# Kernel tuning notes

Hardware: AMD Instinct MI355X
Metric: run time of the kernel (lower is better)

## Reference

```python
import jax, jax.numpy as jnp
import numpy as np

DIM = 512
NUM_HEADS = 16
WIN = (7, 7)
N = WIN[0] * WIN[1]          # 49 tokens per window
NW = 64                      # windows per image
B = 32                       # images
B_ = B * NW                  # total windows = 2048
SCALE = (DIM // NUM_HEADS) ** -0.5


def _relative_position_index(wh, ww):
    coords = np.stack(np.meshgrid(np.arange(wh), np.arange(ww), indexing='ij'))  # (2, wh, ww)
    coords = coords.reshape(2, -1)                                               # (2, N)
    rel = coords[:, :, None] - coords[:, None, :]                                # (2, N, N)
    rel = rel.transpose(1, 2, 0).astype(np.int32)                                # (N, N, 2)
    rel[:, :, 0] += wh - 1
    rel[:, :, 1] += ww - 1
    rel[:, :, 0] *= 2 * ww - 1
    return jnp.asarray(rel.sum(-1), dtype=jnp.int32)                             # (N, N)


def _shift_mask(nw, n):
    # Swin-style additive mask: 0 within groups, -100 across groups.
    rng = np.random.RandomState(0)
    groups = rng.randint(0, 4, size=(nw, n)).astype(np.int32)
    m = np.where(groups[:, :, None] == groups[:, None, :], 0.0, -100.0)
    return jnp.asarray(m, dtype=jnp.float32)                                     # (nW, N, N)


def setup_inputs() -> dict:
    key = jax.random.key(0)
    ks = jax.random.split(key, 5)
    x = jax.random.normal(ks[0], (B_, N, DIM), dtype=jnp.float32)
    qkv_w = jax.random.normal(ks[1], (3 * DIM, DIM), dtype=jnp.float32) * 0.02
    qkv_b = jnp.zeros((3 * DIM,), dtype=jnp.float32)
    proj_w = jax.random.normal(ks[2], (DIM, DIM), dtype=jnp.float32) * 0.02
    proj_b = jnp.zeros((DIM,), dtype=jnp.float32)
    rpb_table = jax.random.normal(ks[3], ((2 * WIN[0] - 1) * (2 * WIN[1] - 1), NUM_HEADS), dtype=jnp.float32) * 0.02
    mask = _shift_mask(NW, N)
    rel_idx = _relative_position_index(*WIN)
    return {"x": x, "mask": mask, "qkv_w": qkv_w, "qkv_b": qkv_b,
            "proj_w": proj_w, "proj_b": proj_b, "rpb_table": rpb_table,
            "rel_idx": rel_idx}


def reference(x, mask, qkv_w, qkv_b, proj_w, proj_b, rpb_table, rel_idx):
    b_, n, c = x.shape
    nh = rpb_table.shape[1]
    d = c // nh
    # qkv projection: (B_, N, 3, nH, d) -> q, k, v each (B_, nH, N, d)
    qkv = (jnp.einsum('bnc,oc->bno', x, qkv_w) + qkv_b).reshape(b_, n, 3, nh, d)
    qkv = jnp.transpose(qkv, (2, 0, 3, 1, 4))
    q, k, v = qkv[0], qkv[1], qkv[2]
    attn = jnp.einsum('bhnd,bhmd->bhnm', q * SCALE, k)                     # (B_, nH, N, N)
    # gathered relative position bias: (N*N, nH) -> (nH, N, N)
    bias = rpb_table[rel_idx.reshape(-1)].reshape(n, n, nh)
    attn = attn + jnp.transpose(bias, (2, 0, 1))[None]
    # shifted-window mask add
    nw = mask.shape[0]
    attn = attn.reshape(b_ // nw, nw, nh, n, n) + mask[None, :, None]
    attn = attn.reshape(b_, nh, n, n)
    attn = jax.nn.softmax(attn, axis=-1)
    out = jnp.einsum('bhnm,bhmd->bhnd', attn, v)                           # (B_, nH, N, d)
    out = jnp.transpose(out, (0, 2, 1, 3)).reshape(b_, n, c)
    return jnp.einsum('bnc,oc->bno', out, proj_w) + proj_b
```

## Files before the change

### kernel.cpp

```cpp
#include <hip/hip_runtime.h>
#include <hip/hip_bf16.h>
#include <stdint.h>
#include <stddef.h>

#define B_TOT   2048
#define NTOK    49
#define CDIM    512
#define NHEAD   16
#define HD      32
#define NWIN    64
#define MROWS   (B_TOT*NTOK)
#define O_QKV   1536
#define SCALE_F 0.17677669529663687f

typedef short bf16x8 __attribute__((ext_vector_type(8)));
typedef float f32x4  __attribute__((ext_vector_type(4)));

__device__ __forceinline__ unsigned short f2bf(float f){
  union { float f; unsigned u; } v; v.f = f;
  unsigned r = v.u + 0x7fffu + ((v.u >> 16) & 1u);
  return (unsigned short)(r >> 16);
}

#define GL16(g,l) __builtin_amdgcn_global_load_lds( \
      (const __attribute__((address_space(1))) unsigned int*)(g), \
      (__attribute__((address_space(3))) unsigned int*)(l), 16, 0, 0)

__global__ void k_cvt_x(const float* __restrict__ x, unsigned short* __restrict__ xb, int n4){
  int i = blockIdx.x * blockDim.x + threadIdx.x;
  int st = gridDim.x * blockDim.x;
  for (; i < n4; i += st){
    float4 v = ((const float4*)x)[i];
    uint2 o;
    o.x = (unsigned)f2bf(v.x) | ((unsigned)f2bf(v.y) << 16);
    o.y = (unsigned)f2bf(v.z) | ((unsigned)f2bf(v.w) << 16);
    ((uint2*)xb)[i] = o;
  }
}

__global__ void k_prep(const float* __restrict__ qkv_w, const float* __restrict__ proj_w,
                       const float* __restrict__ rpb, const int* __restrict__ rel_idx,
                       const float* __restrict__ mask,
                       unsigned short* __restrict__ wqkv, unsigned short* __restrict__ wproj,
                       float* __restrict__ bmb){
  int i = blockIdx.x * blockDim.x + threadIdx.x;
  int st = gridDim.x * blockDim.x;
  for (int j = i; j < O_QKV*CDIM; j += st) wqkv[j] = f2bf(qkv_w[j]);
  for (int j = i; j < CDIM*CDIM;  j += st) wproj[j] = f2bf(proj_w[j]);
  const int TOT = NWIN * NHEAD * NTOK * 64;
  for (int j = i; j < TOT; j += st){
    int wh  = j / (NTOK*64);
    int rem = j - wh * (NTOK*64);
    int qt  = rem >> 6, kt = rem & 63;
    int wi = wh >> 4, h = wh & 15;
    float v;
    if (kt < NTOK){
      int rc = qt * NTOK + kt;
      v = mask[wi * (NTOK*NTOK) + rc] + rpb[rel_idx[rc] * NHEAD + h];
    } else v = -1e30f;
    bmb[j] = v;
  }
}

#define LDA_(P,RG,MI,S) (*(const bf16x8*)(rA + (P)*32768 + (RG)*16384 + (MI)*2048 + ((S)?(cb0^64):cb0)))
#define LDB_(P,CG,NI,S) (*(const bf16x8*)(rB + (P)*32768 + (CG)*16384 + (NI)*2048 + ((S)?(cb0^64):cb0)))

#define STAGE_A(P,HG,KT) { \
    GL16(aS0 + (size_t)(HG)*64*Kb + (size_t)(KT)*128, ldA + (P)*32768 + (HG)*16384); \
    GL16(aS1 + (size_t)(HG)*64*Kb + (size_t)(KT)*128, ldA + (P)*32768 + (HG)*16384 + 8192); }
#define STAGE_B(P,HG,KT) { \
    GL16(bS0 + (size_t)(HG)*32*Kb + (size_t)(KT)*128, ldB + (P)*32768 + (HG)*16384); \
    GL16(bS1 + (size_t)(HG)*32*Kb + (size_t)(KT)*128, ldB + (P)*32768 + (HG)*16384 + 8192); }

#define PHASE(P,RG,CG,DOA,DOB,VM,...) { \
  if (DOA){ _Pragma("unroll") for (int mi=0;mi<4;++mi){ af[mi][0]=LDA_(P,RG,mi,0); af[mi][1]=LDA_(P,RG,mi,1);} } \
  if (DOB){ _Pragma("unroll") for (int ni=0;ni<2;++ni){ bf_[ni][0]=LDB_(P,CG,ni,0); bf_[ni][1]=LDB_(P,CG,ni,1);} } \
  __VA_ARGS__; \
  __builtin_amdgcn_s_barrier(); \
  asm volatile("s_waitcnt lgkmcnt(0)" ::: "memory"); \
  __builtin_amdgcn_sched_barrier(0); \
  __builtin_amdgcn_s_setprio(1); \
  _Pragma("unroll") for (int s=0;s<2;++s) \
    _Pragma("unroll") for (int mi=0;mi<4;++mi) \
      _Pragma("unroll") for (int ni=0;ni<2;++ni) \
        acc[(RG)*4+mi][(CG)*2+ni] = __builtin_amdgcn_mfma_f32_16x16x32_bf16(af[mi][s], bf_[ni][s], acc[(RG)*4+mi][(CG)*2+ni], 0,0,0); \
  __builtin_amdgcn_s_setprio(0); \
  if (VM) asm volatile("s_waitcnt vmcnt(4)" ::: "memory"); \
  __builtin_amdgcn_s_barrier(); \
  asm volatile("" ::: "memory"); \
}

template<int OUT_F32>
__global__ __launch_bounds__(512, 2) void k_gemm8(const unsigned short* __restrict__ Ag,
                                                  const unsigned short* __restrict__ Bg,
                                                  const float* __restrict__ bias,
                                                  void* __restrict__ Cout,
                                                  int Ndim, int Kdim){
  extern __shared__ char smem[];
  const int tid = threadIdx.x;
  const int wv = tid >> 6, lane = tid & 63, lg = lane >> 4, lr = lane & 15;
  const int wm = wv >> 2, wn = wv & 3;

  const int nbx = gridDim.x;
  const int nwg = nbx * gridDim.y;
  const int id  = blockIdx.y * nbx + blockIdx.x;
  const int nid = (id & 7) * (nwg >> 3) + (id >> 3);
  const int bx = nid % nbx, by = nid / nbx;
  const int bm0 = by * 256, bn0 = bx * 256;
  const size_t Kb = (size_t)Kdim * 2;
  const int NIT = Kdim >> 7;

  const int srow = tid >> 3;
  const int scb  = ((tid & 7) << 4) ^ ((srow & 7) << 4);
  const char* aS0 = (const char*)Ag + (size_t)(bm0 + srow) * Kb + scb;
  const char* aS1 = (const char*)Ag + (size_t)(bm0 + 128 + srow) * Kb + scb;
  const char* bS0 = (const char*)Bg + (size_t)(bn0 + (srow>>5)*64 + (srow&31)) * Kb + scb;
  const char* bS1 = (const char*)Bg + (size_t)(bn0 + 128 + (srow>>5)*64 + (srow&31)) * Kb + scb;
  char* ldA = smem + wv * 1024;
  char* ldB = smem + 65536 + wv * 1024;

  const int cb0 = (lg * 16) ^ ((lr & 7) << 4);
  const char* rA = smem + (wm*64 + lr) * 128;
  const char* rB = smem + 65536 + (wn*32 + lr) * 128;

  f32x4 acc[8][4];
  #pragma unroll
  for (int i = 0; i < 8; ++i)
    #pragma unroll
    for (int j = 0; j < 4; ++j)
      #pragma unroll
      for (int r = 0; r < 4; ++r) acc[i][j][r] = 0.f;

  bf16x8 af[4][2], bf_[2][2];

  STAGE_A(0,0,0); STAGE_A(0,1,0); STAGE_B(0,0,0); STAGE_B(0,1,0);
  STAGE_A(1,0,1); STAGE_B(1,1,1);
  asm volatile("s_waitcnt vmcnt(4)" ::: "memory");
  __builtin_amdgcn_s_barrier();
  asm volatile("" ::: "memory");

  for (int it = 0; it < NIT; ++it){
    const int T = 2*it;
    PHASE(0, 0,0, 1,1, 0, STAGE_A(1,1,(T+1)))
    PHASE(0, 0,1, 0,1, 0, STAGE_B(1,0,(T+1)))
    PHASE(0, 1,1, 1,0, 0, STAGE_A(0,0,(T+2)))
    PHASE(0, 1,0, 0,1, 1, STAGE_B(0,1,(T+2)))
    PHASE(1, 0,0, 1,1, 0, STAGE_A(0,1,(T+2)))
    PHASE(1, 0,1, 0,1, 0, STAGE_B(0,0,(T+2)))
    PHASE(1, 1,1, 1,0, 0, STAGE_A(1,0,(T+3)))
    PHASE(1, 1,0, 0,1, 1, STAGE_B(1,1,(T+3)))
  }

  #pragma unroll
  for (int RG = 0; RG < 2; ++RG)
    #pragma unroll
    for (int mi = 0; mi < 4; ++mi)
      #pragma unroll
      for (int CG = 0; CG < 2; ++CG)
        #pragma unroll
        for (int ni = 0; ni < 2; ++ni){
          f32x4 v = acc[RG*4+mi][CG*2+ni];
          const int col = bn0 + wn*64 + CG*32 + ni*16 + lr;
          const float bc = bias[col];
          #pragma unroll
          for (int r = 0; r < 4; ++r){
            const int row = bm0 + wm*128 + RG*64 + mi*16 + lg*4 + r;
            const float t = v[r] + bc;
            if (OUT_F32) ((float*)Cout)[(size_t)row * Ndim + col] = t;
            else ((unsigned short*)Cout)[(size_t)row * Ndim + col] = f2bf(t);
          }
        }
}

__global__ __launch_bounds__(256) void k_attn(const unsigned short* __restrict__ qkv,
                                              const float* __restrict__ bm,
                                              unsigned short* __restrict__ ao){
  __shared__ char lds[4][12288];
  const int wv = threadIdx.x >> 6, lane = threadIdx.x & 63;
  const int lg = lane >> 4, lr = lane & 15;
  const int gw = blockIdx.x * 4 + wv;
  const int w = gw >> 4, h = gw & 15, wi = w & (NWIN - 1);
  char* Vt = lds[wv];
  char* P  = lds[wv] + 4096;

  const unsigned short* base = qkv + (size_t)w * NTOK * O_QKV + h * HD;

  const int vkt = lane >> 2, vch = lane & 3;
  bf16x8 vld[4];
  #pragma unroll
  for (int t = 0; t < 4; ++t){
    int kt = 16*t + vkt; int kts = kt < NTOK ? kt : NTOK-1;
    vld[t] = *(const bf16x8*)(base + 1024 + (size_t)kts * O_QKV + vch * 8);
  }

  bf16x8 qf[4], kf[4];
  #pragma unroll
  for (int i = 0; i < 4; ++i){
    int t = 16*i + lr; int ts = t < NTOK ? t : NTOK-1;
    qf[i] = *(const bf16x8*)(base + (size_t)ts * O_QKV + lg*8);
    kf[i] = *(const bf16x8*)(base + 512 + (size_t)ts * O_QKV + lg*8);
  }

  const float* bmp = bm + (size_t)(wi * NHEAD + h) * (NTOK * 64);
  f32x4 bias[4][4];
  #pragma unroll
  for (int mi = 0; mi < 4; ++mi){
    int qt = 16*mi + lr; int qtc = qt < NTOK ? qt : NTOK-1;
    #pragma unroll
    for (int ni = 0; ni < 4; ++ni)
      bias[mi][ni] = *(const f32x4*)(bmp + qtc*64 + ni*16 + lg*4);
  }

  f32x4 z4 = {0.f, 0.f, 0.f, 0.f};
  f32x4 s2[4][4];
  #pragma unroll
  for (int ni = 0; ni < 4; ++ni)
    #pragma unroll
    for (int mi = 0; mi < 4; ++mi)
      s2[ni][mi] = __builtin_amdgcn_mfma_f32_16x16x32_bf16(kf[ni], qf[mi], z4, 0, 0, 0);

  #pragma unroll
  for (int t = 0; t < 4; ++t){
    int kt = 16*t + vkt;
    #pragma unroll
    for (int j = 0; j < 8; ++j){
      int d = vch*8 + j;
      int swz = ((d & 7) ^ (d >> 3)) & 7;
      int byte = d*128 + ((2*kt) ^ (swz << 4));
      *(unsigned short*)(Vt + byte) = (unsigned short)vld[t][j];
    }
  }

  #pragma unroll
  for (int mi = 0; mi < 4; ++mi){
    float v[4][4];
    float mx = -1e30f;
    #pragma unroll
    for (int ni = 0; ni < 4; ++ni)
      #pragma unroll
      for (int r = 0; r < 4; ++r){
        float t = s2[ni][mi][r] * SCALE_F + bias[mi][ni][r];
        v[ni][r] = t;
        mx = fmaxf(mx, t);
      }
    mx = fmaxf(mx, __shfl_xor(mx, 16));
    mx = fmaxf(mx, __shfl_xor(mx, 32));
    float sum = 0.f;
    #pragma unroll
    for (int ni = 0; ni < 4; ++ni)
      #pragma unroll
      for (int r = 0; r < 4; ++r){
        float p = __expf(v[ni][r] - mx);
        v[ni][r] = p;
        sum += p;
      }
    sum += __shfl_xor(sum, 16);
    sum += __shfl_xor(sum, 32);
    float rn = 1.0f / sum;
    const int qt = 16*mi + lr;
    #pragma unroll
    for (int ni = 0; ni < 4; ++ni){
      unsigned p0 = (unsigned)f2bf(v[ni][0]*rn) | ((unsigned)f2bf(v[ni][1]*rn) << 16);
      unsigned p1 = (unsigned)f2bf(v[ni][2]*rn) | ((unsigned)f2bf(v[ni][3]*rn) << 16);
      uint2 pw; pw.x = p0; pw.y = p1;
      int byte = qt*128 + ((32*ni + 8*lg) ^ ((lr & 7) << 4));
      *(uint2*)(P + byte) = pw;
    }
  }

  f32x4 o[4][2];
  #pragma unroll
  for (int mi = 0; mi < 4; ++mi)
    #pragma unroll
    for (int ni = 0; ni < 2; ++ni)
      #pragma unroll
      for (int r = 0; r < 4; ++r) o[mi][ni][r] = 0.f;

  #pragma unroll
  for (int s = 0; s < 2; ++s){
    bf16x8 pf[4], vf[2];
    #pragma unroll
    for (int mi = 0; mi < 4; ++mi)
      pf[mi] = *(const bf16x8*)(P + (16*mi + lr)*128 + ((64*s + 16*lg) ^ ((lr & 7) << 4)));
    #pragma unroll
    for (int ni = 0; ni < 2; ++ni){
      int d = 16*ni + lr;
      int swz = ((d & 7) ^ (d >> 3)) & 7;
      vf[ni] = *(const bf16x8*)(Vt + d*128 + ((64*s + 16*lg) ^ (swz << 4)));
    }
    #pragma unroll
    for (int mi = 0; mi < 4; ++mi)
      #pragma unroll
      for (int ni = 0; ni < 2; ++ni)
        o[mi][ni] = __builtin_amdgcn_mfma_f32_16x16x32_bf16(pf[mi], vf[ni], o[mi][ni], 0, 0, 0);
  }

  unsigned short* aop = ao + (size_t)w * NTOK * CDIM + h * HD;
  #pragma unroll
  for (int mi = 0; mi < 4; ++mi)
    #pragma unroll
    for (int ni = 0; ni < 2; ++ni)
      #pragma unroll
      for (int r = 0; r < 4; ++r){
        int row = 16*mi + 4*lg + r, col = 16*ni + lr;
        if (row < NTOK)
          aop[(size_t)row * CDIM + col] = f2bf(o[mi][ni][r]);
      }
}

extern "C" void kernel_launch(void* const* d_in, const int* in_sizes, int n_in,
                              void* d_out, int out_size, void* d_ws, size_t ws_size,
                              hipStream_t stream){
  const float* x      = (const float*)d_in[0];
  const float* mask   = (const float*)d_in[1];
  const float* qkv_w  = (const float*)d_in[2];
  const float* qkv_b  = (const float*)d_in[3];
  const float* proj_w = (const float*)d_in[4];
  const float* proj_b = (const float*)d_in[5];
  const float* rpb    = (const float*)d_in[6];
  const int*   rel_i  = (const int*)d_in[7];

  char* ws = (char*)d_ws;
  unsigned short* xb    = (unsigned short*)(ws);
  unsigned short* qkvb  = (unsigned short*)(ws + 102760448);
  unsigned short* wqkv  = (unsigned short*)(ws + 411041792);
  unsigned short* wproj = (unsigned short*)(ws + 412614656);
  float*          bmb   = (float*)(ws + 413138944);

  (void)hipFuncSetAttribute(reinterpret_cast<const void*>(&k_gemm8<0>),
                            hipFuncAttributeMaxDynamicSharedMemorySize, 131072);
  (void)hipFuncSetAttribute(reinterpret_cast<const void*>(&k_gemm8<1>),
                            hipFuncAttributeMaxDynamicSharedMemorySize, 131072);

  k_cvt_x<<<2048, 256, 0, stream>>>(x, xb, MROWS * CDIM / 4);
  k_prep<<<512, 256, 0, stream>>>(qkv_w, proj_w, rpb, rel_i, mask, wqkv, wproj, bmb);
  k_gemm8<0><<<dim3(O_QKV/256, MROWS/256), 512, 131072, stream>>>(xb, wqkv, qkv_b, qkvb, O_QKV, CDIM);
  k_attn<<<(B_TOT * NHEAD) / 4, 256, 0, stream>>>(qkvb, bmb, xb);
  k_gemm8<1><<<dim3(CDIM/256, MROWS/256), 512, 131072, stream>>>(xb, wproj, proj_b, d_out, CDIM, CDIM);
}
```

Before: 505.2 us.

## Fuse fp32-to-bf16 conversion of x into the QKV GEMM A-operand loads

Drops the separate x conversion kernel and adds a QKV GEMM variant that reads fp32 x directly into registers, converts to bf16 and writes it to LDS itself, while B still streams through direct global-to-LDS loads. This removes one full read and write pass over the 100MB activation buffer plus a kernel launch. The cost is that the GEMM now reads twice the bytes for A through registers with a reworked pipeline schedule, which adds register pressure and VALU work in the main loop.

New measurement: 596.6 us. 1.18x slower.

```diff
diff --git a/kernel.cpp b/kernel.cpp
--- a/kernel.cpp
+++ b/kernel.cpp
@@ -21,22 +21,13 @@
   unsigned r = v.u + 0x7fffu + ((v.u >> 16) & 1u);
   return (unsigned short)(r >> 16);
 }
+__device__ __forceinline__ unsigned pkbf(float a, float b){
+  return (unsigned)f2bf(a) | ((unsigned)f2bf(b) << 16);
+}
 
 #define GL16(g,l) __builtin_amdgcn_global_load_lds( \
       (const __attribute__((address_space(1))) unsigned int*)(g), \
       (__attribute__((address_space(3))) unsigned int*)(l), 16, 0, 0)
-
-__global__ void k_cvt_x(const float* __restrict__ x, unsigned short* __restrict__ xb, int n4){
-  int i = blockIdx.x * blockDim.x + threadIdx.x;
-  int st = gridDim.x * blockDim.x;
-  for (; i < n4; i += st){
-    float4 v = ((const float4*)x)[i];
-    uint2 o;
-    o.x = (unsigned)f2bf(v.x) | ((unsigned)f2bf(v.y) << 16);
-    o.y = (unsigned)f2bf(v.z) | ((unsigned)f2bf(v.w) << 16);
-    ((uint2*)xb)[i] = o;
-  }
-}
 
 __global__ void k_prep(const float* __restrict__ qkv_w, const float* __restrict__ proj_w,
                        const float* __restrict__ rpb, const int* __restrict__ rel_idx,
@@ -65,6 +56,133 @@
 #define LDA_(P,RG,MI,S) (*(const bf16x8*)(rA + (P)*32768 + (RG)*16384 + (MI)*2048 + ((S)?(cb0^64):cb0)))
 #define LDB_(P,CG,NI,S) (*(const bf16x8*)(rB + (P)*32768 + (CG)*16384 + (NI)*2048 + ((S)?(cb0^64):cb0)))
 
+#define RDA(P,RG) { _Pragma("unroll") for (int mi=0;mi<4;++mi){ af[mi][0]=LDA_(P,RG,mi,0); af[mi][1]=LDA_(P,RG,mi,1);} }
+#define RDB0(P,CG) { _Pragma("unroll") for (int ni=0;ni<2;++ni){ bfr0[ni][0]=LDB_(P,CG,ni,0); bfr0[ni][1]=LDB_(P,CG,ni,1);} }
+#define RDB1(P,CG) { _Pragma("unroll") for (int ni=0;ni<2;++ni){ bfr1[ni][0]=LDB_(P,CG,ni,0); bfr1[ni][1]=LDB_(P,CG,ni,1);} }
+
+#define IA(SET,HG,KT) { \
+  const int kc_ = (KT) < NK ? (KT) : 0; \
+  const float4* _p = xrow + (size_t)(HG)*64*F4row + kc_*16; \
+  ia##SET[0] = _p[0]; ia##SET[1] = _p[1]; \
+  const float4* _q = _p + (size_t)128*F4row; \
+  ia##SET[2] = _q[0]; ia##SET[3] = _q[1]; }
+
+#define WA(SET,P,HG) { \
+  uint4 _w; \
+  _w.x = pkbf(ia##SET[0].x, ia##SET[0].y); _w.y = pkbf(ia##SET[0].z, ia##SET[0].w); \
+  _w.z = pkbf(ia##SET[1].x, ia##SET[1].y); _w.w = pkbf(ia##SET[1].z, ia##SET[1].w); \
+  *(uint4*)(wrA + (P)*32768 + (HG)*16384) = _w; \
+  _w.x = pkbf(ia##SET[2].x, ia##SET[2].y); _w.y = pkbf(ia##SET[2].z, ia##SET[2].w); \
+  _w.z = pkbf(ia##SET[3].x, ia##SET[3].y); _w.w = pkbf(ia##SET[3].z, ia##SET[3].w); \
+  *(uint4*)(wrA + (P)*32768 + (HG)*16384 + 8192) = _w; }
+
+#define SB(P,HG,KT) { \
+    GL16(bS0 + (size_t)(HG)*32*Kb + (size_t)(KT)*128, ldB + (P)*32768 + (HG)*16384); \
+    GL16(bS1 + (size_t)(HG)*32*Kb + (size_t)(KT)*128, ldB + (P)*32768 + (HG)*16384 + 8192); }
+
+#define PH(PRE,RG,CG,BF,VM) { \
+  PRE; \
+  __builtin_amdgcn_s_barrier(); \
+  asm volatile("s_waitcnt lgkmcnt(0)" ::: "memory"); \
+  __builtin_amdgcn_sched_barrier(0); \
+  __builtin_amdgcn_s_setprio(1); \
+  _Pragma("unroll") for (int s=0;s<2;++s) \
+    _Pragma("unroll") for (int mi=0;mi<4;++mi) \
+      _Pragma("unroll") for (int ni=0;ni<2;++ni) \
+        acc[(RG)*4+mi][(CG)*2+ni] = __builtin_amdgcn_mfma_f32_16x16x32_bf16(af[mi][s], BF[ni][s], acc[(RG)*4+mi][(CG)*2+ni], 0,0,0); \
+  __builtin_amdgcn_s_setprio(0); \
+  if (VM) asm volatile("s_waitcnt vmcnt(6)" ::: "memory"); \
+  __builtin_amdgcn_s_barrier(); \
+  asm volatile("" ::: "memory"); \
+}
+
+__global__ __launch_bounds__(512, 2) void k_gemmA(const float* __restrict__ Xg,
+                                                  const unsigned short* __restrict__ Bg,
+                                                  const float* __restrict__ bias,
+                                                  unsigned short* __restrict__ Cout,
+                                                  int Ndim, int Kdim){
+  extern __shared__ char smem[];
+  const int tid = threadIdx.x;
+  const int wv = tid >> 6, lane = tid & 63, lg = lane >> 4, lr = lane & 15;
+  const int wm = wv >> 2, wn = wv & 3;
+
+  const int nbx = gridDim.x;
+  const int nwg = nbx * gridDim.y;
+  const int id  = blockIdx.y * nbx + blockIdx.x;
+  const int nid = (id & 7) * (nwg >> 3) + (id >> 3);
+  const int bx = nid % nbx, by = nid / nbx;
+  const int bm0 = by * 256, bn0 = bx * 256;
+  const size_t Kb = (size_t)Kdim * 2;
+  const int F4row = Kdim >> 2;
+  const int NK = Kdim >> 6;
+  const int NIT = Kdim >> 7;
+
+  const int srow = tid >> 3;
+  const float4* xrow = (const float4*)Xg + (size_t)(bm0 + srow) * F4row + (tid & 7) * 2;
+  char* wrA = smem + srow*128 + (((tid & 7) << 4) ^ ((srow & 7) << 4));
+  const int scb = ((tid & 7) << 4) ^ ((srow & 7) << 4);
+  const char* bS0 = (const char*)Bg + (size_t)(bn0 + (srow>>5)*64 + (srow&31)) * Kb + scb;
+  const char* bS1 = (const char*)Bg + (size_t)(bn0 + 128 + (srow>>5)*64 + (srow&31)) * Kb + scb;
+  char* ldB = smem + 65536 + wv * 1024;
+
+  const int cb0 = (lg * 16) ^ ((lr & 7) << 4);
+  const char* rA = smem + (wm*64 + lr) * 128;
+  const char* rB = smem + 65536 + (wn*32 + lr) * 128;
+
+  f32x4 acc[8][4];
+  #pragma unroll
+  for (int i = 0; i < 8; ++i)
+    #pragma unroll
+    for (int j = 0; j < 4; ++j)
+      #pragma unroll
+      for (int r = 0; r < 4; ++r) acc[i][j][r] = 0.f;
+
+  bf16x8 af[4][2], bfr0[2][2], bfr1[2][2];
+  float4 ia0[4], ia1[4];
+
+  IA(0, 0, 0);
+  IA(1, 1, 0);
+  SB(0, 0, 0);
+  SB(0, 1, 0);
+  WA(0, 0, 0);
+  WA(1, 0, 1);
+  IA(0, 0, 1);
+  SB(1, 1, 1);
+  asm volatile("s_waitcnt vmcnt(6)" ::: "memory");
+  __builtin_amdgcn_s_barrier();
+  asm volatile("" ::: "memory");
+
+  for (int it = 0; it < NIT; ++it){
+    const int T = 2*it;
+    PH( IA(1,1,(T+1)); RDA(0,0); RDB0(0,0); WA(0,1,0), 0,0, bfr0, 0)
+    PH( SB(1,0,(T+1)); RDB1(0,1),                      0,1, bfr1, 0)
+    PH( IA(0,0,(T+2)); RDA(0,1); WA(1,1,1),            1,1, bfr1, 0)
+    PH( SB(0,1,(T+2)),                                 1,0, bfr0, 1)
+    PH( IA(1,1,(T+2)); RDA(1,0); RDB0(1,0); WA(0,0,0), 0,0, bfr0, 0)
+    PH( SB(0,0,(T+2)); RDB1(1,1),                      0,1, bfr1, 0)
+    PH( IA(0,0,(T+3)); RDA(1,1); WA(1,0,1),            1,1, bfr1, 0)
+    PH( SB(1,1,(T+3)),                                 1,0, bfr0, 1)
+  }
+
+  #pragma unroll
+  for (int RG = 0; RG < 2; ++RG)
+    #pragma unroll
+    for (int mi = 0; mi < 4; ++mi)
+      #pragma unroll
+      for (int CG = 0; CG < 2; ++CG)
+        #pragma unroll
+        for (int ni = 0; ni < 2; ++ni){
+          f32x4 v = acc[RG*4+mi][CG*2+ni];
+          const int col = bn0 + wn*64 + CG*32 + ni*16 + lr;
+          const float bc = bias[col];
+          #pragma unroll
+          for (int r = 0; r < 4; ++r){
+            const int row = bm0 + wm*128 + RG*64 + mi*16 + lg*4 + r;
+            Cout[(size_t)row * Ndim + col] = f2bf(v[r] + bc);
+          }
+        }
+}
+
 #define STAGE_A(P,HG,KT) { \
     GL16(aS0 + (size_t)(HG)*64*Kb + (size_t)(KT)*128, ldA + (P)*32768 + (HG)*16384); \
     GL16(aS1 + (size_t)(HG)*64*Kb + (size_t)(KT)*128, ldA + (P)*32768 + (HG)*16384 + 8192); }
@@ -90,11 +208,10 @@
   asm volatile("" ::: "memory"); \
 }
 
-template<int OUT_F32>
 __global__ __launch_bounds__(512, 2) void k_gemm8(const unsigned short* __restrict__ Ag,
                                                   const unsigned short* __restrict__ Bg,
                                                   const float* __restrict__ bias,
-                                                  void* __restrict__ Cout,
+                                                  float* __restrict__ Cout,
                                                   int Ndim, int Kdim){
   extern __shared__ char smem[];
   const int tid = threadIdx.x;
@@ -165,9 +282,7 @@
           #pragma unroll
           for (int r = 0; r < 4; ++r){
             const int row = bm0 + wm*128 + RG*64 + mi*16 + lg*4 + r;
-            const float t = v[r] + bc;
-            if (OUT_F32) ((float*)Cout)[(size_t)row * Ndim + col] = t;
-            else ((unsigned short*)Cout)[(size_t)row * Ndim + col] = f2bf(t);
+            Cout[(size_t)row * Ndim + col] = v[r] + bc;
           }
         }
 }
@@ -321,20 +436,19 @@
   const int*   rel_i  = (const int*)d_in[7];
 
   char* ws = (char*)d_ws;
-  unsigned short* xb    = (unsigned short*)(ws);
+  unsigned short* aob   = (unsigned short*)(ws);
   unsigned short* qkvb  = (unsigned short*)(ws + 102760448);
   unsigned short* wqkv  = (unsigned short*)(ws + 411041792);
   unsigned short* wproj = (unsigned short*)(ws + 412614656);
   float*          bmb   = (float*)(ws + 413138944);
 
-  (void)hipFuncSetAttribute(reinterpret_cast<const void*>(&k_gemm8<0>),
+  (void)hipFuncSetAttribute(reinterpret_cast<const void*>(&k_gemmA),
                             hipFuncAttributeMaxDynamicSharedMemorySize, 131072);
-  (void)hipFuncSetAttribute(reinterpret_cast<const void*>(&k_gemm8<1>),
+  (void)hipFuncSetAttribute(reinterpret_cast<const void*>(&k_gemm8),
                             hipFuncAttributeMaxDynamicSharedMemorySize, 131072);
 
-  k_cvt_x<<<2048, 256, 0, stream>>>(x, xb, MROWS * CDIM / 4);
   k_prep<<<512, 256, 0, stream>>>(qkv_w, proj_w, rpb, rel_i, mask, wqkv, wproj, bmb);
-  k_gemm8<0><<<dim3(O_QKV/256, MROWS/256), 512, 131072, stream>>>(xb, wqkv, qkv_b, qkvb, O_QKV, CDIM);
-  k_attn<<<(B_TOT * NHEAD) / 4, 256, 0, stream>>>(qkvb, bmb, xb);
-  k_gemm8<1><<<dim3(CDIM/256, MROWS/256), 512, 131072, stream>>>(xb, wproj, proj_b, d_out, CDIM, CDIM);
-}
+  k_gemmA<<<dim3(O_QKV/256, MROWS/256), 512, 131072, stream>>>(x, wqkv, qkv_b, qkvb, O_QKV, CDIM);
+  k_attn<<<(B_TOT * NHEAD) / 4, 256, 0, stream>>>(qkvb, bmb, aob);
+  k_gemm8<<<dim3(CDIM/256, MROWS/256), 512, 131072, stream>>>(aob, wproj, proj_b, (float*)d_out, CDIM, CDIM);
+}
```

## Fuse window attention with output projection in one per-window kernel

Applied to the files above, without the earlier changes.

Replaces the separate attention kernel and output-projection GEMM with one kernel where each block handles a whole window. Each of its 4 waves computes 4 heads and stages the bf16 attention output in LDS, then the block multiplies it by the projection weights read directly from global memory. This removes the bf16 attention-output round trip through HBM and one launch. In exchange the projection uses a simple unpipelined GEMM that reloads weights per window from L2, with 64-row tiles padded from 49 rows, and the large LDS footprint may limit occupancy.

Result: slower. 573.8 us (+13.6%).

```diff
diff --git a/kernel.cpp b/kernel.cpp
--- a/kernel.cpp
+++ b/kernel.cpp
@@ -20,6 +20,9 @@
   union { float f; unsigned u; } v; v.f = f;
   unsigned r = v.u + 0x7fffu + ((v.u >> 16) & 1u);
   return (unsigned short)(r >> 16);
+}
+__device__ __forceinline__ unsigned pkbf(float a, float b){
+  return (unsigned)f2bf(a) | ((unsigned)f2bf(b) << 16);
 }
 
 #define GL16(g,l) __builtin_amdgcn_global_load_lds( \
@@ -90,11 +93,10 @@
   asm volatile("" ::: "memory"); \
 }
 
-template<int OUT_F32>
 __global__ __launch_bounds__(512, 2) void k_gemm8(const unsigned short* __restrict__ Ag,
                                                   const unsigned short* __restrict__ Bg,
                                                   const float* __restrict__ bias,
-                                                  void* __restrict__ Cout,
+                                                  unsigned short* __restrict__ Cout,
                                                   int Ndim, int Kdim){
   extern __shared__ char smem[];
   const int tid = threadIdx.x;
@@ -165,147 +167,188 @@
           #pragma unroll
           for (int r = 0; r < 4; ++r){
             const int row = bm0 + wm*128 + RG*64 + mi*16 + lg*4 + r;
-            const float t = v[r] + bc;
-            if (OUT_F32) ((float*)Cout)[(size_t)row * Ndim + col] = t;
-            else ((unsigned short*)Cout)[(size_t)row * Ndim + col] = f2bf(t);
+            Cout[(size_t)row * Ndim + col] = f2bf(v[r] + bc);
           }
         }
 }
 
-__global__ __launch_bounds__(256) void k_attn(const unsigned short* __restrict__ qkv,
-                                              const float* __restrict__ bm,
-                                              unsigned short* __restrict__ ao){
-  __shared__ char lds[4][12288];
+__global__ __launch_bounds__(256) void k_attnproj(const unsigned short* __restrict__ qkv,
+                                                  const float* __restrict__ bm,
+                                                  const unsigned short* __restrict__ wproj,
+                                                  const float* __restrict__ projb,
+                                                  float* __restrict__ out){
+  extern __shared__ char lds[];
   const int wv = threadIdx.x >> 6, lane = threadIdx.x & 63;
   const int lg = lane >> 4, lr = lane & 15;
-  const int gw = blockIdx.x * 4 + wv;
-  const int w = gw >> 4, h = gw & 15, wi = w & (NWIN - 1);
-  char* Vt = lds[wv];
-  char* P  = lds[wv] + 4096;
-
-  const unsigned short* base = qkv + (size_t)w * NTOK * O_QKV + h * HD;
+  const int w = blockIdx.x, wi = w & (NWIN - 1);
+  char* AO = lds;
+  char* Vt = lds + 65536 + wv * 12288;
+  char* P  = Vt + 4096;
 
   const int vkt = lane >> 2, vch = lane & 3;
-  bf16x8 vld[4];
-  #pragma unroll
-  for (int t = 0; t < 4; ++t){
-    int kt = 16*t + vkt; int kts = kt < NTOK ? kt : NTOK-1;
-    vld[t] = *(const bf16x8*)(base + 1024 + (size_t)kts * O_QKV + vch * 8);
-  }
-
-  bf16x8 qf[4], kf[4];
-  #pragma unroll
-  for (int i = 0; i < 4; ++i){
-    int t = 16*i + lr; int ts = t < NTOK ? t : NTOK-1;
-    qf[i] = *(const bf16x8*)(base + (size_t)ts * O_QKV + lg*8);
-    kf[i] = *(const bf16x8*)(base + 512 + (size_t)ts * O_QKV + lg*8);
-  }
-
-  const float* bmp = bm + (size_t)(wi * NHEAD + h) * (NTOK * 64);
-  f32x4 bias[4][4];
-  #pragma unroll
-  for (int mi = 0; mi < 4; ++mi){
-    int qt = 16*mi + lr; int qtc = qt < NTOK ? qt : NTOK-1;
+  f32x4 z4 = {0.f, 0.f, 0.f, 0.f};
+
+  #pragma unroll
+  for (int hi = 0; hi < 4; ++hi){
+    const int h = wv*4 + hi;
+    const unsigned short* base = qkv + (size_t)w * NTOK * O_QKV + h * HD;
+
+    bf16x8 vld[4];
+    #pragma unroll
+    for (int t = 0; t < 4; ++t){
+      int kt = 16*t + vkt; int kts = kt < NTOK ? kt : NTOK-1;
+      vld[t] = *(const bf16x8*)(base + 1024 + (size_t)kts * O_QKV + vch * 8);
+    }
+    bf16x8 qf[4], kf[4];
+    #pragma unroll
+    for (int i = 0; i < 4; ++i){
+      int t = 16*i + lr; int ts = t < NTOK ? t : NTOK-1;
+      qf[i] = *(const bf16x8*)(base + (size_t)ts * O_QKV + lg*8);
+      kf[i] = *(const bf16x8*)(base + 512 + (size_t)ts * O_QKV + lg*8);
+    }
+    const float* bmp = bm + (size_t)(wi * NHEAD + h) * (NTOK * 64);
+    f32x4 bias[4][4];
+    #pragma unroll
+    for (int mi = 0; mi < 4; ++mi){
+      int qt = 16*mi + lr; int qtc = qt < NTOK ? qt : NTOK-1;
+      #pragma unroll
+      for (int ni = 0; ni < 4; ++ni)
+        bias[mi][ni] = *(const f32x4*)(bmp + qtc*64 + ni*16 + lg*4);
+    }
+    f32x4 s2[4][4];
     #pragma unroll
     for (int ni = 0; ni < 4; ++ni)
-      bias[mi][ni] = *(const f32x4*)(bmp + qtc*64 + ni*16 + lg*4);
-  }
-
-  f32x4 z4 = {0.f, 0.f, 0.f, 0.f};
-  f32x4 s2[4][4];
-  #pragma unroll
-  for (int ni = 0; ni < 4; ++ni)
+      #pragma unroll
+      for (int mi = 0; mi < 4; ++mi)
+        s2[ni][mi] = __builtin_amdgcn_mfma_f32_16x16x32_bf16(kf[ni], qf[mi], z4, 0, 0, 0);
+
+    #pragma unroll
+    for (int t = 0; t < 4; ++t){
+      int kt = 16*t + vkt;
+      #pragma unroll
+      for (int j = 0; j < 8; ++j){
+        int d = vch*8 + j;
+        int swz = ((d & 7) ^ (d >> 3)) & 7;
+        *(unsigned short*)(Vt + d*128 + ((2*kt) ^ (swz << 4))) = (unsigned short)vld[t][j];
+      }
+    }
+    #pragma unroll
+    for (int mi = 0; mi < 4; ++mi){
+      float v[4][4];
+      float mx = -1e30f;
+      #pragma unroll
+      for (int ni = 0; ni < 4; ++ni)
+        #pragma unroll
+        for (int r = 0; r < 4; ++r){
+          float t = s2[ni][mi][r] * SCALE_F + bias[mi][ni][r];
+          v[ni][r] = t;
+          mx = fmaxf(mx, t);
+        }
+      mx = fmaxf(mx, __shfl_xor(mx, 16));
+      mx = fmaxf(mx, __shfl_xor(mx, 32));
+      float sum = 0.f;
+      #pragma unroll
+      for (int ni = 0; ni < 4; ++ni)
+        #pragma unroll
+        for (int r = 0; r < 4; ++r){
+          float p = __expf(v[ni][r] - mx);
+          v[ni][r] = p;
+          sum += p;
+        }
+      sum += __shfl_xor(sum, 16);
+      sum += __shfl_xor(sum, 32);
+      float rn = 1.0f / sum;
+      const int qt = 16*mi + lr;
+      #pragma unroll
+      for (int ni = 0; ni < 4; ++ni){
+        uint2 pw;
+        pw.x = pkbf(v[ni][0]*rn, v[ni][1]*rn);
+        pw.y = pkbf(v[ni][2]*rn, v[ni][3]*rn);
+        *(uint2*)(P + qt*128 + ((32*ni + 8*lg) ^ ((lr & 7) << 4))) = pw;
+      }
+    }
+    f32x4 ot[2][4];
+    #pragma unroll
+    for (int mi = 0; mi < 2; ++mi)
+      #pragma unroll
+      for (int nj = 0; nj < 4; ++nj)
+        #pragma unroll
+        for (int r = 0; r < 4; ++r) ot[mi][nj][r] = 0.f;
+
+    #pragma unroll
+    for (int s = 0; s < 2; ++s){
+      bf16x8 vf[2], pfb[4];
+      #pragma unroll
+      for (int mi = 0; mi < 2; ++mi){
+        int d = 16*mi + lr;
+        int swz = ((d & 7) ^ (d >> 3)) & 7;
+        vf[mi] = *(const bf16x8*)(Vt + d*128 + ((64*s + 16*lg) ^ (swz << 4)));
+      }
+      #pragma unroll
+      for (int nj = 0; nj < 4; ++nj){
+        int qt = 16*nj + lr;
+        pfb[nj] = *(const bf16x8*)(P + qt*128 + ((64*s + 16*lg) ^ ((lr & 7) << 4)));
+      }
+      #pragma unroll
+      for (int mi = 0; mi < 2; ++mi)
+        #pragma unroll
+        for (int nj = 0; nj < 4; ++nj)
+          ot[mi][nj] = __builtin_amdgcn_mfma_f32_16x16x32_bf16(vf[mi], pfb[nj], ot[mi][nj], 0, 0, 0);
+    }
+    #pragma unroll
+    for (int mi = 0; mi < 2; ++mi){
+      const int colb = h*32 + 16*mi + 4*lg;
+      #pragma unroll
+      for (int nj = 0; nj < 4; ++nj){
+        const int qt = 16*nj + lr;
+        uint2 pw;
+        pw.x = pkbf(ot[mi][nj][0], ot[mi][nj][1]);
+        pw.y = pkbf(ot[mi][nj][2], ot[mi][nj][3]);
+        *(uint2*)(AO + qt*1024 + ((2*colb) ^ ((qt & 7) << 4))) = pw;
+      }
+    }
+  }
+  __syncthreads();
+
+  const int N0 = wv * 128;
+  f32x4 pacc[4][8];
+  #pragma unroll
+  for (int mi = 0; mi < 4; ++mi)
+    #pragma unroll
+    for (int ni = 0; ni < 8; ++ni)
+      #pragma unroll
+      for (int r = 0; r < 4; ++r) pacc[mi][ni][r] = 0.f;
+
+  for (int ks = 0; ks < 16; ++ks){
+    bf16x8 bfrag[8], afrag[4];
+    #pragma unroll
+    for (int ni = 0; ni < 8; ++ni)
+      bfrag[ni] = *(const bf16x8*)(wproj + (size_t)(N0 + 16*ni + lr) * CDIM + ks*32 + lg*8);
+    #pragma unroll
+    for (int mi = 0; mi < 4; ++mi){
+      int row = 16*mi + lr;
+      afrag[mi] = *(const bf16x8*)(AO + row*1024 + ((ks*64 + 16*lg) ^ ((lr & 7) << 4)));
+    }
     #pragma unroll
     for (int mi = 0; mi < 4; ++mi)
-      s2[ni][mi] = __builtin_amdgcn_mfma_f32_16x16x32_bf16(kf[ni], qf[mi], z4, 0, 0, 0);
-
-  #pragma unroll
-  for (int t = 0; t < 4; ++t){
-    int kt = 16*t + vkt;
-    #pragma unroll
-    for (int j = 0; j < 8; ++j){
-      int d = vch*8 + j;
-      int swz = ((d & 7) ^ (d >> 3)) & 7;
-      int byte = d*128 + ((2*kt) ^ (swz << 4));
-      *(unsigned short*)(Vt + byte) = (unsigned short)vld[t][j];
-    }
-  }
-
-  #pragma unroll
-  for (int mi = 0; mi < 4; ++mi){
-    float v[4][4];
-    float mx = -1e30f;
-    #pragma unroll
-    for (int ni = 0; ni < 4; ++ni)
+      #pragma unroll
+      for (int ni = 0; ni < 8; ++ni)
+        pacc[mi][ni] = __builtin_amdgcn_mfma_f32_16x16x32_bf16(afrag[mi], bfrag[ni], pacc[mi][ni], 0, 0, 0);
+  }
+
+  float* orow = out + (size_t)w * NTOK * CDIM;
+  #pragma unroll
+  for (int mi = 0; mi < 4; ++mi)
+    #pragma unroll
+    for (int ni = 0; ni < 8; ++ni){
+      const int col = N0 + 16*ni + lr;
+      const float bc = projb[col];
       #pragma unroll
       for (int r = 0; r < 4; ++r){
-        float t = s2[ni][mi][r] * SCALE_F + bias[mi][ni][r];
-        v[ni][r] = t;
-        mx = fmaxf(mx, t);
-      }
-    mx = fmaxf(mx, __shfl_xor(mx, 16));
-    mx = fmaxf(mx, __shfl_xor(mx, 32));
-    float sum = 0.f;
-    #pragma unroll
-    for (int ni = 0; ni < 4; ++ni)
-      #pragma unroll
-      for (int r = 0; r < 4; ++r){
-        float p = __expf(v[ni][r] - mx);
-        v[ni][r] = p;
-        sum += p;
-      }
-    sum += __shfl_xor(sum, 16);
-    sum += __shfl_xor(sum, 32);
-    float rn = 1.0f / sum;
-    const int qt = 16*mi + lr;
-    #pragma unroll
-    for (int ni = 0; ni < 4; ++ni){
-      unsigned p0 = (unsigned)f2bf(v[ni][0]*rn) | ((unsigned)f2bf(v[ni][1]*rn) << 16);
-      unsigned p1 = (unsigned)f2bf(v[ni][2]*rn) | ((unsigned)f2bf(v[ni][3]*rn) << 16);
-      uint2 pw; pw.x = p0; pw.y = p1;
-      int byte = qt*128 + ((32*ni + 8*lg) ^ ((lr & 7) << 4));
-      *(uint2*)(P + byte) = pw;
-    }
-  }
-
-  f32x4 o[4][2];
-  #pragma unroll
-  for (int mi = 0; mi < 4; ++mi)
-    #pragma unroll
-    for (int ni = 0; ni < 2; ++ni)
-      #pragma unroll
-      for (int r = 0; r < 4; ++r) o[mi][ni][r] = 0.f;
-
-  #pragma unroll
-  for (int s = 0; s < 2; ++s){
-    bf16x8 pf[4], vf[2];
-    #pragma unroll
-    for (int mi = 0; mi < 4; ++mi)
-      pf[mi] = *(const bf16x8*)(P + (16*mi + lr)*128 + ((64*s + 16*lg) ^ ((lr & 7) << 4)));
-    #pragma unroll
-    for (int ni = 0; ni < 2; ++ni){
-      int d = 16*ni + lr;
-      int swz = ((d & 7) ^ (d >> 3)) & 7;
-      vf[ni] = *(const bf16x8*)(Vt + d*128 + ((64*s + 16*lg) ^ (swz << 4)));
-    }
-    #pragma unroll
-    for (int mi = 0; mi < 4; ++mi)
-      #pragma unroll
-      for (int ni = 0; ni < 2; ++ni)
-        o[mi][ni] = __builtin_amdgcn_mfma_f32_16x16x32_bf16(pf[mi], vf[ni], o[mi][ni], 0, 0, 0);
-  }
-
-  unsigned short* aop = ao + (size_t)w * NTOK * CDIM + h * HD;
-  #pragma unroll
-  for (int mi = 0; mi < 4; ++mi)
-    #pragma unroll
-    for (int ni = 0; ni < 2; ++ni)
-      #pragma unroll
-      for (int r = 0; r < 4; ++r){
-        int row = 16*mi + 4*lg + r, col = 16*ni + lr;
-        if (row < NTOK)
-          aop[(size_t)row * CDIM + col] = f2bf(o[mi][ni][r]);
-      }
+        const int row = 16*mi + 4*lg + r;
+        if (row < NTOK) orow[(size_t)row * CDIM + col] = pacc[mi][ni][r] + bc;
+      }
+    }
 }
 
 extern "C" void kernel_launch(void* const* d_in, const int* in_sizes, int n_in,
@@ -327,14 +370,13 @@
   unsigned short* wproj = (unsigned short*)(ws + 412614656);
   float*          bmb   = (float*)(ws + 413138944);
 
-  (void)hipFuncSetAttribute(reinterpret_cast<const void*>(&k_gemm8<0>),
+  (void)hipFuncSetAttribute(reinterpret_cast<const void*>(&k_gemm8),
                             hipFuncAttributeMaxDynamicSharedMemorySize, 131072);
-  (void)hipFuncSetAttribute(reinterpret_cast<const void*>(&k_gemm8<1>),
-                            hipFuncAttributeMaxDynamicSharedMemorySize, 131072);
+  (void)hipFuncSetAttribute(reinterpret_cast<const void*>(&k_attnproj),
+                            hipFuncAttributeMaxDynamicSharedMemorySize, 114688);
 
   k_cvt_x<<<2048, 256, 0, stream>>>(x, xb, MROWS * CDIM / 4);
   k_prep<<<512, 256, 0, stream>>>(qkv_w, proj_w, rpb, rel_i, mask, wqkv, wproj, bmb);
-  k_gemm8<0><<<dim3(O_QKV/256, MROWS/256), 512, 131072, stream>>>(xb, wqkv, qkv_b, qkvb, O_QKV, CDIM);
-  k_attn<<<(B_TOT * NHEAD) / 4, 256, 0, stream>>>(qkvb, bmb, xb);
-  k_gemm8<1><<<dim3(CDIM/256, MROWS/256), 512, 131072, stream>>>(xb, wproj, proj_b, d_out, CDIM, CDIM);
-}
+  k_gemm8<<<dim3(O_QKV/256, MROWS/256), 512, 131072, stream>>>(xb, wqkv, qkv_b, qkvb, O_QKV, CDIM);
+  k_attnproj<<<B_TOT, 256, 114688, stream>>>(qkvb, bmb, wproj, proj_b, (float*)d_out);
+}
```
